# Kernel optimization log

Measured on AMD Instinct MI355X. Metric: run time of the kernel, lower is better.

The kernel has to match this reference:

```python
import jax, jax.numpy as jnp
import numpy as np

N_NODES = 50000
N_EDGES = 800000
D_IN = 128
D_SH = 16
D_OUT = 128
N_PATHS = 64


def setup_inputs() -> dict:
    key = jax.random.key(0)
    k1, k2, k3, k4, k5, k6, k7, k8 = jax.random.split(key, 8)
    x = jax.random.normal(k1, (N_NODES, D_IN), dtype=jnp.float32)
    sh = jax.random.normal(k2, (N_EDGES, D_SH), dtype=jnp.float32)
    coeff = jax.random.normal(k3, (N_PATHS,), dtype=jnp.float32)
    src = jax.random.randint(k4, (N_EDGES,), 0, N_NODES, dtype=jnp.int64)
    dst = jax.random.randint(k5, (N_EDGES,), 0, N_NODES, dtype=jnp.int64)
    ki = jax.random.randint(k6, (N_PATHS,), 0, D_IN, dtype=jnp.int32)
    kj = jax.random.randint(k7, (N_PATHS,), 0, D_SH, dtype=jnp.int32)
    ko = jax.random.randint(k8, (N_PATHS,), 0, D_OUT, dtype=jnp.int32)
    return {"x": x, "sh": sh, "coeff": coeff, "src": src, "dst": dst,
            "ki": ki, "kj": kj, "ko": ko}


def reference(x, sh, coeff, src, dst, ki, kj, ko):
    # 1) gather: index_select node features by edge source -> [E, D_in]
    xg = x[src]
    # 2) segmented tensor product: sum over sparse paths p of
    #    coeff[p] * xg[:, ki[p]] * sh[:, kj[p]] accumulated into output slot ko[p]
    vals = coeff[None, :] * xg[:, ki] * sh[:, kj]          # [E, P]
    msg = jnp.zeros((sh.shape[0], D_OUT), dtype=x.dtype).at[:, ko].add(vals)  # [E, D_out]
    # 3) scatter_add messages into per-node output -> [N, D_out]
    out = jnp.zeros((x.shape[0], D_OUT), dtype=x.dtype).at[dst].add(msg)
    return out
```

## Files before the change

kernel.cpp:

```cpp
#include <hip/hip_runtime.h>
#include <hip/hip_fp16.h>

#define N_NODES 50000
#define N_EDGES 800000
#define D_IN    128
#define D_SH    16
#define D_OUT   128
#define N_PATHS 64

#define SEGN    128
#define NSEG    391
#define NSEGP   512
#define CAPE    2560
#define EPB     3125
#define BINB    256
#define XCB     3125
#define BLK     256

#define QN      16
#define QCAP    512
#define NQB     (NSEG * 8)
#define SCAN_K  10

#define OFF_META 2048
#define OFF_SH16 (OFF_META + NSEG*CAPE*4)
#define OFF_XCH  (OFF_SH16 + NSEG*CAPE*32)

__global__ __launch_bounds__(BLK) void bin_kernel(
        const float* __restrict__ x, const int* __restrict__ ki,
        const float* __restrict__ sh, const int* __restrict__ src,
        const int* __restrict__ dst, int* __restrict__ segcnt,
        int* __restrict__ meta, __half* __restrict__ sh16,
        __half* __restrict__ xc_h) {
    __shared__ int lcnt[NSEGP];
    __shared__ int lstart[NSEGP];
    __shared__ int lofs[NSEGP];
    __shared__ int gbase[NSEGP];
    __shared__ unsigned short sorted_[EPB];
    const int tid = threadIdx.x;

    if (blockIdx.x < BINB) {
        const int e0 = blockIdx.x * EPB;
        for (int s = tid; s < NSEGP; s += BLK) lcnt[s] = 0;
        __syncthreads();
        for (int i = tid; i < EPB; i += BLK)
            atomicAdd(&lcnt[dst[e0 + i] >> 7], 1);
        __syncthreads();
        if (tid < 64) {
            int b8 = tid * 8, v[8], s0 = 0;
            #pragma unroll
            for (int k = 0; k < 8; ++k) { v[k] = lcnt[b8 + k]; s0 += v[k]; }
            int run = s0;
            #pragma unroll
            for (int off = 1; off < 64; off <<= 1) {
                int y = __shfl_up(run, off);
                if (tid >= off) run += y;
            }
            int acc = run - s0;
            #pragma unroll
            for (int k = 0; k < 8; ++k) {
                lstart[b8 + k] = acc; lofs[b8 + k] = acc; acc += v[k];
            }
        } else {
            for (int s = tid - 64; s < NSEG; s += BLK - 64) {
                int c = lcnt[s];
                gbase[s] = c ? atomicAdd(&segcnt[s], c) : 0;
            }
        }
        __syncthreads();
        for (int i = tid; i < EPB; i += BLK) {
            int r = atomicAdd(&lofs[dst[e0 + i] >> 7], 1);
            sorted_[r] = (unsigned short)i;
        }
        __syncthreads();
        for (int j = tid; j < EPB; j += BLK) {
            int i = sorted_[j];
            int e = e0 + i;
            int d = dst[e];
            int s = d >> 7;
            int pos = gbase[s] + (j - lstart[s]);
            if (pos < CAPE) {
                size_t gi = (size_t)s * CAPE + pos;
                meta[gi] = src[e] | ((d & 127) << 16);
                const float4* shv = (const float4*)(sh + (size_t)e * D_SH);
                float4 f0 = shv[0], f1 = shv[1], f2 = shv[2], f3 = shv[3];
                union { __half2 h[8]; int4 v[2]; } u;
                u.h[0] = __floats2half2_rn(f0.x, f0.y);
                u.h[1] = __floats2half2_rn(f0.z, f0.w);
                u.h[2] = __floats2half2_rn(f1.x, f1.y);
                u.h[3] = __floats2half2_rn(f1.z, f1.w);
                u.h[4] = __floats2half2_rn(f2.x, f2.y);
                u.h[5] = __floats2half2_rn(f2.z, f2.w);
                u.h[6] = __floats2half2_rn(f3.x, f3.y);
                u.h[7] = __floats2half2_rn(f3.z, f3.w);
                int4* dp = (int4*)(sh16 + gi * 16);
                dp[0] = u.v[0]; dp[1] = u.v[1];
            }
        }
    } else {
        const int b2   = blockIdx.x - BINB;
        const int lane = tid & 63;
        const int w    = tid >> 6;
        const int nb   = b2 * 16 + w * 4;
        const int kil  = ki[lane];
        float x0 = x[(size_t)(nb + 0) * D_IN + kil];
        float x1 = x[(size_t)(nb + 1) * D_IN + kil];
        float x2 = x[(size_t)(nb + 2) * D_IN + kil];
        float x3 = x[(size_t)(nb + 3) * D_IN + kil];
        xc_h[(size_t)(nb + 0) * N_PATHS + lane] = __float2half_rn(x0);
        xc_h[(size_t)(nb + 1) * N_PATHS + lane] = __float2half_rn(x1);
        xc_h[(size_t)(nb + 2) * N_PATHS + lane] = __float2half_rn(x2);
        xc_h[(size_t)(nb + 3) * N_PATHS + lane] = __float2half_rn(x3);
    }
}

__global__ __launch_bounds__(BLK) void node_kernel(
        const int* __restrict__ segcnt, const int* __restrict__ meta,
        const __half* __restrict__ sh16, const __half* __restrict__ xc_h,
        const float* __restrict__ coeff, const int* __restrict__ kj,
        const int* __restrict__ ko, float* __restrict__ out) {
    __shared__ int cnt_l[QN];
    __shared__ int nstart[QN + 1];
    __shared__ int ncur[QN];
    __shared__ unsigned short csr_src[QCAP];
    __shared__ unsigned short csr_idx[QCAP];
    __shared__ float srow[BLK / 64][4][D_OUT];
    const int tid  = threadIdx.x;
    const int lane = tid & 63;
    const int w    = tid >> 6;
    const int seg  = blockIdx.x >> 3;
    const int q    = blockIdx.x & 7;
    const int nb_l = q * QN;
    const int n_e  = min(segcnt[seg], CAPE);
    const size_t mb = (size_t)seg * CAPE;
    const __half* shb = sh16 + mb * 16;

    if (tid < QN) cnt_l[tid] = 0;
    __syncthreads();

    int mreg[SCAN_K];
    #pragma unroll
    for (int k = 0; k < SCAN_K; ++k) {
        int i = tid + k * BLK;
        int m = (i < n_e) ? meta[mb + i] : -1;
        mreg[k] = m;
        unsigned int u = (unsigned)(((m >> 16) & 127) - nb_l);
        if (i < n_e && u < QN) atomicAdd(&cnt_l[u], 1);
    }
    __syncthreads();
    if (tid < QN) {
        int v = cnt_l[tid];
        int run = v;
        #pragma unroll
        for (int off = 1; off < QN; off <<= 1) {
            int y = __shfl_up(run, off);
            if (tid >= off) run += y;
        }
        nstart[tid] = run - v;
        ncur[tid]   = run - v;
        if (tid == QN - 1) nstart[QN] = run;
    }
    __syncthreads();
    #pragma unroll
    for (int k = 0; k < SCAN_K; ++k) {
        int i = tid + k * BLK;
        int m = mreg[k];
        unsigned int u = (unsigned)(((m >> 16) & 127) - nb_l);
        if (i < n_e && u < QN) {
            int r = atomicAdd(&ncur[u], 1);
            if (r < QCAP) {
                csr_src[r] = (unsigned short)(m & 0xFFFF);
                csr_idx[r] = (unsigned short)i;
            }
        }
    }
    __syncthreads();

    const int   kj_p = kj[lane];
    const int   ko_p = ko[lane];
    const float c_p  = coeff[lane];

    float accs[4];
    #pragma unroll
    for (int c4 = 0; c4 < 4; ++c4) {
        const int c  = w * 4 + c4;
        const int st = min(nstart[c], QCAP);
        const int en = min(nstart[c + 1], QCAP);
        float acc = 0.0f;
        int j = st;
        for (; j + 16 <= en; j += 16) {
            float xv[16], sv[16];
            #pragma unroll
            for (int u8 = 0; u8 < 16; ++u8) {
                int s = csr_src[j + u8];
                int i = csr_idx[j + u8];
                xv[u8] = __half2float(xc_h[(size_t)s * N_PATHS + lane]);
                sv[u8] = __half2float(shb[(size_t)i * 16 + kj_p]);
            }
            #pragma unroll
            for (int u8 = 0; u8 < 16; ++u8) acc += xv[u8] * sv[u8];
        }
        if (j < en) {
            float xv[16], sv[16];
            #pragma unroll
            for (int u8 = 0; u8 < 16; ++u8) {
                int jj = j + u8;
                int jc = jj < en ? jj : st;
                int s = csr_src[jc];
                int i = csr_idx[jc];
                xv[u8] = __half2float(xc_h[(size_t)s * N_PATHS + lane]);
                sv[u8] = __half2float(shb[(size_t)i * 16 + kj_p]);
            }
            #pragma unroll
            for (int u8 = 0; u8 < 16; ++u8)
                if (j + u8 < en) acc += xv[u8] * sv[u8];
        }
        accs[c4] = acc * c_p;
    }

    #pragma unroll
    for (int c4 = 0; c4 < 4; ++c4) {
        srow[w][c4][lane]      = 0.0f;
        srow[w][c4][lane + 64] = 0.0f;
    }
    #pragma unroll
    for (int c4 = 0; c4 < 4; ++c4)
        atomicAdd(&srow[w][c4][ko_p], accs[c4]);
    #pragma unroll
    for (int c4 = 0; c4 < 4; ++c4) {
        const int node = seg * SEGN + nb_l + w * 4 + c4;
        if (node < N_NODES) {
            float r0 = srow[w][c4][lane];
            float r1 = srow[w][c4][lane + 64];
            float* orow = out + (size_t)node * D_OUT;
            orow[lane]      = r0;
            orow[lane + 64] = r1;
        }
    }
}

extern "C" void kernel_launch(void* const* d_in, const int* in_sizes, int n_in,
                              void* d_out, int out_size, void* d_ws, size_t ws_size,
                              hipStream_t stream) {
    const float* x     = (const float*)d_in[0];
    const float* sh    = (const float*)d_in[1];
    const float* coeff = (const float*)d_in[2];
    const int*   src   = (const int*)d_in[3];
    const int*   dst   = (const int*)d_in[4];
    const int*   ki    = (const int*)d_in[5];
    const int*   kj    = (const int*)d_in[6];
    const int*   ko    = (const int*)d_in[7];
    float* out = (float*)d_out;

    char* p = (char*)d_ws;
    int*    segcnt = (int*)p;
    int*    meta   = (int*)(p + OFF_META);
    __half* sh16   = (__half*)(p + OFF_SH16);
    __half* xc_h   = (__half*)(p + OFF_XCH);
    (void)ws_size;

    hipMemsetAsync(segcnt, 0, 2048, stream);
    bin_kernel<<<BINB + XCB, BLK, 0, stream>>>(
        x, ki, sh, src, dst, segcnt, meta, sh16, xc_h);
    node_kernel<<<NQB, BLK, 0, stream>>>(
        segcnt, meta, sh16, xc_h, coeff, kj, ko, out);
}
```

Baseline: 216.2 us.

## Use persistent work-queue node kernel with 32-node units and LDS-staged meta

Replaces the one-block-per-quarter-segment grid with a persistent grid of blocks that pull work units from a global atomic counter. Each unit now covers 32 nodes (4 units per segment instead of 8), which halves how many times each segment's meta list is rescanned. The meta is staged into shared memory (aliased over srow) instead of being held in registers. The aim is to cut redundant meta reads and balance load, at the cost of a global atomic per unit, more shared memory, and fewer parallel units.

```diff
diff --git a/kernel.cpp b/kernel.cpp
--- a/kernel.cpp
+++ b/kernel.cpp
@@ -17,11 +17,12 @@
 #define XCB     3125
 #define BLK     256
 
-#define QN      16
-#define QCAP    512
-#define NQB     (NSEG * 8)
-#define SCAN_K  10
-
+#define QN      32
+#define QCAP    1024
+#define NUNITS  (NSEG * 4)
+#define NGRID   2048
+
+#define OFF_QH   1600
 #define OFF_META 2048
 #define OFF_SH16 (OFF_META + NSEG*CAPE*4)
 #define OFF_XCH  (OFF_SH16 + NSEG*CAPE*32)
@@ -118,123 +119,126 @@
         const int* __restrict__ segcnt, const int* __restrict__ meta,
         const __half* __restrict__ sh16, const __half* __restrict__ xc_h,
         const float* __restrict__ coeff, const int* __restrict__ kj,
-        const int* __restrict__ ko, float* __restrict__ out) {
+        const int* __restrict__ ko, int* __restrict__ qhead,
+        float* __restrict__ out) {
+    __shared__ float srow[BLK / 64][8][D_OUT];
+    int* metash = (int*)&srow[0][0][0];
+    __shared__ unsigned short csr_src[QCAP];
+    __shared__ unsigned short csr_idx[QCAP];
     __shared__ int cnt_l[QN];
     __shared__ int nstart[QN + 1];
     __shared__ int ncur[QN];
-    __shared__ unsigned short csr_src[QCAP];
-    __shared__ unsigned short csr_idx[QCAP];
-    __shared__ float srow[BLK / 64][4][D_OUT];
+    __shared__ int qunit;
     const int tid  = threadIdx.x;
     const int lane = tid & 63;
     const int w    = tid >> 6;
-    const int seg  = blockIdx.x >> 3;
-    const int q    = blockIdx.x & 7;
-    const int nb_l = q * QN;
-    const int n_e  = min(segcnt[seg], CAPE);
-    const size_t mb = (size_t)seg * CAPE;
-    const __half* shb = sh16 + mb * 16;
-
-    if (tid < QN) cnt_l[tid] = 0;
-    __syncthreads();
-
-    int mreg[SCAN_K];
-    #pragma unroll
-    for (int k = 0; k < SCAN_K; ++k) {
-        int i = tid + k * BLK;
-        int m = (i < n_e) ? meta[mb + i] : -1;
-        mreg[k] = m;
-        unsigned int u = (unsigned)(((m >> 16) & 127) - nb_l);
-        if (i < n_e && u < QN) atomicAdd(&cnt_l[u], 1);
-    }
-    __syncthreads();
-    if (tid < QN) {
-        int v = cnt_l[tid];
-        int run = v;
-        #pragma unroll
-        for (int off = 1; off < QN; off <<= 1) {
-            int y = __shfl_up(run, off);
-            if (tid >= off) run += y;
-        }
-        nstart[tid] = run - v;
-        ncur[tid]   = run - v;
-        if (tid == QN - 1) nstart[QN] = run;
-    }
-    __syncthreads();
-    #pragma unroll
-    for (int k = 0; k < SCAN_K; ++k) {
-        int i = tid + k * BLK;
-        int m = mreg[k];
-        unsigned int u = (unsigned)(((m >> 16) & 127) - nb_l);
-        if (i < n_e && u < QN) {
-            int r = atomicAdd(&ncur[u], 1);
-            if (r < QCAP) {
-                csr_src[r] = (unsigned short)(m & 0xFFFF);
-                csr_idx[r] = (unsigned short)i;
-            }
-        }
-    }
-    __syncthreads();
 
     const int   kj_p = kj[lane];
     const int   ko_p = ko[lane];
     const float c_p  = coeff[lane];
 
-    float accs[4];
-    #pragma unroll
-    for (int c4 = 0; c4 < 4; ++c4) {
-        const int c  = w * 4 + c4;
-        const int st = min(nstart[c], QCAP);
-        const int en = min(nstart[c + 1], QCAP);
-        float acc = 0.0f;
-        int j = st;
-        for (; j + 16 <= en; j += 16) {
-            float xv[16], sv[16];
-            #pragma unroll
-            for (int u8 = 0; u8 < 16; ++u8) {
-                int s = csr_src[j + u8];
-                int i = csr_idx[j + u8];
-                xv[u8] = __half2float(xc_h[(size_t)s * N_PATHS + lane]);
-                sv[u8] = __half2float(shb[(size_t)i * 16 + kj_p]);
-            }
-            #pragma unroll
-            for (int u8 = 0; u8 < 16; ++u8) acc += xv[u8] * sv[u8];
-        }
-        if (j < en) {
-            float xv[16], sv[16];
-            #pragma unroll
-            for (int u8 = 0; u8 < 16; ++u8) {
-                int jj = j + u8;
-                int jc = jj < en ? jj : st;
-                int s = csr_src[jc];
-                int i = csr_idx[jc];
-                xv[u8] = __half2float(xc_h[(size_t)s * N_PATHS + lane]);
-                sv[u8] = __half2float(shb[(size_t)i * 16 + kj_p]);
-            }
-            #pragma unroll
-            for (int u8 = 0; u8 < 16; ++u8)
-                if (j + u8 < en) acc += xv[u8] * sv[u8];
-        }
-        accs[c4] = acc * c_p;
-    }
-
-    #pragma unroll
-    for (int c4 = 0; c4 < 4; ++c4) {
-        srow[w][c4][lane]      = 0.0f;
-        srow[w][c4][lane + 64] = 0.0f;
-    }
-    #pragma unroll
-    for (int c4 = 0; c4 < 4; ++c4)
-        atomicAdd(&srow[w][c4][ko_p], accs[c4]);
-    #pragma unroll
-    for (int c4 = 0; c4 < 4; ++c4) {
-        const int node = seg * SEGN + nb_l + w * 4 + c4;
-        if (node < N_NODES) {
-            float r0 = srow[w][c4][lane];
-            float r1 = srow[w][c4][lane + 64];
-            float* orow = out + (size_t)node * D_OUT;
-            orow[lane]      = r0;
-            orow[lane + 64] = r1;
+    for (;;) {
+        if (tid == 0) qunit = atomicAdd(qhead, 1);
+        if (tid < QN) cnt_l[tid] = 0;
+        __syncthreads();
+        const int unit = qunit;
+        if (unit >= NUNITS) return;
+
+        const int seg  = unit >> 2;
+        const int nb_l = (unit & 3) * QN;
+        const int n_e  = min(segcnt[seg], CAPE);
+        const size_t mb = (size_t)seg * CAPE;
+        const __half* shb = sh16 + mb * 16;
+
+        for (int i = tid; i < n_e; i += BLK) {
+            int m = meta[mb + i];
+            metash[i] = m;
+            unsigned int u = (unsigned)(((m >> 16) & 127) - nb_l);
+            if (u < QN) atomicAdd(&cnt_l[u], 1);
+        }
+        __syncthreads();
+        if (tid < QN) {
+            int v = cnt_l[tid];
+            int run = v;
+            #pragma unroll
+            for (int off = 1; off < QN; off <<= 1) {
+                int y = __shfl_up(run, off);
+                if (tid >= off) run += y;
+            }
+            nstart[tid] = run - v;
+            ncur[tid]   = run - v;
+            if (tid == QN - 1) nstart[QN] = run;
+        }
+        __syncthreads();
+        for (int i = tid; i < n_e; i += BLK) {
+            int m = metash[i];
+            unsigned int u = (unsigned)(((m >> 16) & 127) - nb_l);
+            if (u < QN) {
+                int r = atomicAdd(&ncur[u], 1);
+                if (r < QCAP) {
+                    csr_src[r] = (unsigned short)(m & 0xFFFF);
+                    csr_idx[r] = (unsigned short)i;
+                }
+            }
+        }
+        __syncthreads();
+
+        float accs[8];
+        #pragma unroll
+        for (int c8 = 0; c8 < 8; ++c8) {
+            const int c  = w * 8 + c8;
+            const int st = min(nstart[c], QCAP);
+            const int en = min(nstart[c + 1], QCAP);
+            float acc = 0.0f;
+            int j = st;
+            for (; j + 16 <= en; j += 16) {
+                float xv[16], sv[16];
+                #pragma unroll
+                for (int u8 = 0; u8 < 16; ++u8) {
+                    int s = csr_src[j + u8];
+                    int i = csr_idx[j + u8];
+                    xv[u8] = __half2float(xc_h[(size_t)s * N_PATHS + lane]);
+                    sv[u8] = __half2float(shb[(size_t)i * 16 + kj_p]);
+                }
+                #pragma unroll
+                for (int u8 = 0; u8 < 16; ++u8) acc += xv[u8] * sv[u8];
+            }
+            if (j < en) {
+                float xv[16], sv[16];
+                #pragma unroll
+                for (int u8 = 0; u8 < 16; ++u8) {
+                    int jj = j + u8;
+                    int jc = jj < en ? jj : st;
+                    int s = csr_src[jc];
+                    int i = csr_idx[jc];
+                    xv[u8] = __half2float(xc_h[(size_t)s * N_PATHS + lane]);
+                    sv[u8] = __half2float(shb[(size_t)i * 16 + kj_p]);
+                }
+                #pragma unroll
+                for (int u8 = 0; u8 < 16; ++u8)
+                    if (j + u8 < en) acc += xv[u8] * sv[u8];
+            }
+            accs[c8] = acc * c_p;
+        }
+
+        #pragma unroll
+        for (int c8 = 0; c8 < 8; ++c8) {
+            srow[w][c8][lane]      = 0.0f;
+            srow[w][c8][lane + 64] = 0.0f;
+        }
+        #pragma unroll
+        for (int c8 = 0; c8 < 8; ++c8)
+            atomicAdd(&srow[w][c8][ko_p], accs[c8]);
+        #pragma unroll
+        for (int c8 = 0; c8 < 8; ++c8) {
+            const int node = seg * SEGN + nb_l + w * 8 + c8;
+            if (node < N_NODES) {
+                float r0 = srow[w][c8][lane];
+                float r1 = srow[w][c8][lane + 64];
+                float* orow = out + (size_t)node * D_OUT;
+                orow[lane]      = r0;
+                orow[lane + 64] = r1;
+            }
         }
     }
 }
@@ -254,14 +258,15 @@
 
     char* p = (char*)d_ws;
     int*    segcnt = (int*)p;
+    int*    qhead  = (int*)(p + OFF_QH);
     int*    meta   = (int*)(p + OFF_META);
     __half* sh16   = (__half*)(p + OFF_SH16);
     __half* xc_h   = (__half*)(p + OFF_XCH);
     (void)ws_size;
 
-    hipMemsetAsync(segcnt, 0, 2048, stream);
+    hipMemsetAsync(p, 0, 2048, stream);
     bin_kernel<<<BINB + XCB, BLK, 0, stream>>>(
         x, ki, sh, src, dst, segcnt, meta, sh16, xc_h);
-    node_kernel<<<NQB, BLK, 0, stream>>>(
-        segcnt, meta, sh16, xc_h, coeff, kj, ko, out);
+    node_kernel<<<NGRID, BLK, 0, stream>>>(
+        segcnt, meta, sh16, xc_h, coeff, kj, ko, qhead, out);
 }
```

Result: slower. 238.7 us (+10.4%).
